# Kernel optimization log

Hardware: AMD Instinct MI355X
Metric: run time of the kernel (lower is better)

## Reference

```python
import jax, jax.numpy as jnp
import numpy as np

HDIM = 4
P = 2 ** HDIM  # 16 hypercube nodes


def build_dense_weight(hweight, out_features, in_features):
    # hweight: [hdim+1, P, ob, ib]; assemble dense [out_features, in_features]
    ob = out_features // P
    ib = in_features // P
    i = jnp.arange(P)
    w = jnp.zeros((P, P, ob, ib), dtype=hweight.dtype)
    # diagonal blocks: w[i, i] = hweight[0, i]
    w = w.at[i, i].set(hweight[0])
    # hypercube neighbor blocks: w[i ^ (1<<d), i] = hweight[d+1, i]
    for d in range(HDIM):
        j = i ^ (1 << d)
        w = w.at[j, i].set(hweight[d + 1])
    # permute (0,2,1,3) then reshape -> [out_features, in_features]
    w = jnp.transpose(w, (0, 2, 1, 3)).reshape(out_features, in_features)
    return w


def setup_inputs() -> dict:
    key = jax.random.key(0)
    k1, k2, k3 = jax.random.split(key, 3)
    in_features, out_features = 4096, 4096
    ob = out_features // P
    ib = in_features // P
    x = jax.random.normal(k1, (8192, in_features), dtype=jnp.float32)
    # kaiming-uniform-like scale for the block weights
    bound_w = 1.0 / np.sqrt(ib)
    hweight = jax.random.uniform(k2, (HDIM + 1, P, ob, ib), dtype=jnp.float32,
                                 minval=-bound_w, maxval=bound_w)
    bound_b = 1.0 / np.sqrt(in_features * (HDIM + 1))
    hbias = jax.random.uniform(k3, (out_features,), dtype=jnp.float32,
                               minval=-bound_b, maxval=bound_b)
    return {"x": x, "hweight": hweight, "hbias": hbias}


def reference(x, hweight, hbias):
    out_features = hweight.shape[1] * hweight.shape[2]
    in_features = hweight.shape[1] * hweight.shape[3]
    w = build_dense_weight(hweight, out_features, in_features)
    # F.linear(x, w, b) = x @ w.T + b
    return x @ w.T + hbias
```

## Files before the change

### kernel.cpp

```cpp
#include <hip/hip_runtime.h>

typedef __attribute__((ext_vector_type(8))) short short8;
typedef __attribute__((ext_vector_type(4))) float f32x4;

#define BM 128
#define BN 128
#define BK 32
#define INF 4096

#define AS1 __attribute__((address_space(1)))
#define AS3 __attribute__((address_space(3)))

__device__ __forceinline__ unsigned short f2bf(float f) {
    unsigned int u = __float_as_uint(f);
    u += 0x7FFFu + ((u >> 16) & 1u);
    return (unsigned short)(u >> 16);
}

__device__ __forceinline__ void gl_lds16(const unsigned short* g, unsigned short* l) {
    __builtin_amdgcn_global_load_lds((const AS1 void*)g, (AS3 void*)l, 16, 0, 0);
}

__global__ __launch_bounds__(256)
void cvt_bf16(const float* __restrict__ x, const float* __restrict__ hw,
              unsigned short* __restrict__ xb, unsigned short* __restrict__ wb)
{
    const long long NX = 8192LL * 4096;
    const long long NW = 5LL * 16 * 256 * 256;
    const long long total8 = (NX + NW) / 8;
    for (long long i = (long long)blockIdx.x * 256 + threadIdx.x; i < total8;
         i += (long long)gridDim.x * 256) {
        long long e = i * 8;
        const float* src;
        unsigned short* dst;
        long long off;
        if (e < NX) { src = x;  dst = xb; off = e; }
        else        { src = hw; dst = wb; off = e - NX; }
        float4 f0 = *(const float4*)(src + off);
        float4 f1 = *(const float4*)(src + off + 4);
        ushort4 u0, u1;
        u0.x = f2bf(f0.x); u0.y = f2bf(f0.y); u0.z = f2bf(f0.z); u0.w = f2bf(f0.w);
        u1.x = f2bf(f1.x); u1.y = f2bf(f1.y); u1.z = f2bf(f1.z); u1.w = f2bf(f1.w);
        *(ushort4*)(dst + off)     = u0;
        *(ushort4*)(dst + off + 4) = u1;
    }
}

__global__ __launch_bounds__(256)
void hcl_gemm(const unsigned short* __restrict__ xb,
              const unsigned short* __restrict__ wb,
              const float* __restrict__ hb,
              float* __restrict__ out)
{
    __shared__ unsigned short As[BM][BK];
    __shared__ unsigned short Bs[BN][BK];

    const int tid  = threadIdx.x;
    const int lane = tid & 63;
    const int wave = tid >> 6;
    const int wr   = wave >> 1, wc = wave & 1;

    const int bm0 = blockIdx.x * BM;
    const int p   = blockIdx.y >> 1;
    const int nh  = blockIdx.y & 1;

    f32x4 acc[4][4] = {};

    const int srow = tid >> 2;
    const int scol = (lane & 3) * 8;
    unsigned short* ldsA0 = &As[wave * 16][0];
    unsigned short* ldsA1 = &As[64 + wave * 16][0];
    unsigned short* ldsB0 = &Bs[wave * 16][0];
    unsigned short* ldsB1 = &Bs[64 + wave * 16][0];

    #pragma unroll
    for (int t = 0; t < 5; ++t) {
        const int mask = (t == 0) ? 0 : (1 << (t - 1));
        const int s = p ^ mask;
        const unsigned short* xc = xb + (size_t)bm0 * INF + s * 256;
        const unsigned short* wc_ = wb + ((size_t)(t * 16 + s) * 256 + nh * 128) * 256;

        for (int k8 = 0; k8 < 8; ++k8) {
            const int kc = k8 * BK;

            gl_lds16(xc  + (size_t)srow        * INF + kc + scol, ldsA0);
            gl_lds16(xc  + (size_t)(64 + srow) * INF + kc + scol, ldsA1);
            gl_lds16(wc_ + (size_t)srow        * 256 + kc + scol, ldsB0);
            gl_lds16(wc_ + (size_t)(64 + srow) * 256 + kc + scol, ldsB1);

            __syncthreads();

            short8 a[4], b[4];
            #pragma unroll
            for (int mi = 0; mi < 4; ++mi)
                a[mi] = *(const short8*)&As[wr * 64 + mi * 16 + (lane & 15)][(lane >> 4) * 8];
            #pragma unroll
            for (int nj = 0; nj < 4; ++nj)
                b[nj] = *(const short8*)&Bs[wc * 64 + nj * 16 + (lane & 15)][(lane >> 4) * 8];

            #pragma unroll
            for (int mi = 0; mi < 4; ++mi)
                #pragma unroll
                for (int nj = 0; nj < 4; ++nj)
                    acc[mi][nj] = __builtin_amdgcn_mfma_f32_16x16x32_bf16(
                        a[mi], b[nj], acc[mi][nj], 0, 0, 0);

            __syncthreads();
        }
    }

    const int col0 = p * 256 + nh * 128 + wc * 64;
    #pragma unroll
    for (int nj = 0; nj < 4; ++nj) {
        const int col = col0 + nj * 16 + (lane & 15);
        const float bias = hb[col];
        #pragma unroll
        for (int mi = 0; mi < 4; ++mi) {
            #pragma unroll
            for (int r = 0; r < 4; ++r) {
                const int row = bm0 + wr * 64 + mi * 16 + (lane >> 4) * 4 + r;
                out[(size_t)row * 4096 + col] = acc[mi][nj][r] + bias;
            }
        }
    }
}

__global__ __launch_bounds__(256)
void hcl_mfma_fused(const float* __restrict__ x,
                    const float* __restrict__ hw,
                    const float* __restrict__ hb,
                    float* __restrict__ out)
{
    __shared__ unsigned short As[BM][BK];
    __shared__ unsigned short Bs[BN][BK];

    const int tid  = threadIdx.x;
    const int lane = tid & 63;
    const int wave = tid >> 6;
    const int wr   = wave >> 1, wc = wave & 1;

    const int bm0 = blockIdx.x * BM;
    const int p   = blockIdx.y >> 1;
    const int nh  = blockIdx.y & 1;

    f32x4 acc[4][4] = {};

    const int srow = tid >> 3;
    const int scol = (tid & 7) * 4;

    #pragma unroll
    for (int t = 0; t < 5; ++t) {
        const int mask = (t == 0) ? 0 : (1 << (t - 1));
        const int s = p ^ mask;
        const float* xchunk = x  + (size_t)bm0 * INF + s * 256;
        const float* wchunk = hw + ((size_t)(t * 16 + s) * 256 + nh * 128) * 256;

        for (int k8 = 0; k8 < 8; ++k8) {
            const int kc = k8 * BK;
            #pragma unroll
            for (int i = 0; i < 4; ++i) {
                const int row = i * 32 + srow;
                float4 fa = *(const float4*)(xchunk + (size_t)row * INF + kc + scol);
                float4 fb = *(const float4*)(wchunk + (size_t)row * 256 + kc + scol);
                ushort4 ua, ub;
                ua.x = f2bf(fa.x); ua.y = f2bf(fa.y);
                ua.z = f2bf(fa.z); ua.w = f2bf(fa.w);
                ub.x = f2bf(fb.x); ub.y = f2bf(fb.y);
                ub.z = f2bf(fb.z); ub.w = f2bf(fb.w);
                *(ushort4*)&As[row][scol] = ua;
                *(ushort4*)&Bs[row][scol] = ub;
            }
            __syncthreads();

            short8 a[4], b[4];
            #pragma unroll
            for (int mi = 0; mi < 4; ++mi)
                a[mi] = *(const short8*)&As[wr * 64 + mi * 16 + (lane & 15)][(lane >> 4) * 8];
            #pragma unroll
            for (int nj = 0; nj < 4; ++nj)
                b[nj] = *(const short8*)&Bs[wc * 64 + nj * 16 + (lane & 15)][(lane >> 4) * 8];

            #pragma unroll
            for (int mi = 0; mi < 4; ++mi)
                #pragma unroll
                for (int nj = 0; nj < 4; ++nj)
                    acc[mi][nj] = __builtin_amdgcn_mfma_f32_16x16x32_bf16(
                        a[mi], b[nj], acc[mi][nj], 0, 0, 0);

            __syncthreads();
        }
    }

    const int col0 = p * 256 + nh * 128 + wc * 64;
    #pragma unroll
    for (int nj = 0; nj < 4; ++nj) {
        const int col = col0 + nj * 16 + (lane & 15);
        const float bias = hb[col];
        #pragma unroll
        for (int mi = 0; mi < 4; ++mi) {
            #pragma unroll
            for (int r = 0; r < 4; ++r) {
                const int row = bm0 + wr * 64 + mi * 16 + (lane >> 4) * 4 + r;
                out[(size_t)row * 4096 + col] = acc[mi][nj][r] + bias;
            }
        }
    }
}

extern "C" void kernel_launch(void* const* d_in, const int* in_sizes, int n_in,
                              void* d_out, int out_size, void* d_ws, size_t ws_size,
                              hipStream_t stream) {
    const float* x  = (const float*)d_in[0];
    const float* hw = (const float*)d_in[1];
    const float* hb = (const float*)d_in[2];
    float* out = (float*)d_out;

    const size_t NX = 8192ull * 4096;
    const size_t NW = 5ull * 16 * 256 * 256;
    const size_t need = (NX + NW) * sizeof(unsigned short);

    if (ws_size >= need) {
        unsigned short* xb = (unsigned short*)d_ws;
        unsigned short* wb = xb + NX;
        cvt_bf16<<<2048, 256, 0, stream>>>(x, hw, xb, wb);
        dim3 grid(8192 / BM, 32);
        hcl_gemm<<<grid, 256, 0, stream>>>(xb, wb, hb, out);
    } else {
        dim3 grid(8192 / BM, 32);
        hcl_mfma_fused<<<grid, 256, 0, stream>>>(x, hw, hb, out);
    }
}
```

Baseline: 169.2 us.

## Rewrite bf16 GEMM with 256x256 tiles, triple-buffered LDS and swizzle

```diff
diff --git a/kernel.cpp b/kernel.cpp
--- a/kernel.cpp
+++ b/kernel.cpp
@@ -3,10 +3,9 @@
 typedef __attribute__((ext_vector_type(8))) short short8;
 typedef __attribute__((ext_vector_type(4))) float f32x4;
 
-#define BM 128
-#define BN 128
-#define BK 32
 #define INF 4096
+#define NKT 40
+#define BUFB 32768
 
 #define AS1 __attribute__((address_space(1)))
 #define AS3 __attribute__((address_space(3)))
@@ -17,9 +16,11 @@
     return (unsigned short)(u >> 16);
 }
 
-__device__ __forceinline__ void gl_lds16(const unsigned short* g, unsigned short* l) {
+__device__ __forceinline__ void gl_lds16(const unsigned short* g, void* l) {
     __builtin_amdgcn_global_load_lds((const AS1 void*)g, (AS3 void*)l, 16, 0, 0);
 }
+
+__device__ __forceinline__ int swz(int b) { return b ^ ((b >> 3) & 0x30); }
 
 __global__ __launch_bounds__(256)
 void cvt_bf16(const float* __restrict__ x, const float* __restrict__ hw,
@@ -46,80 +47,108 @@
     }
 }
 
-__global__ __launch_bounds__(256)
-void hcl_gemm(const unsigned short* __restrict__ xb,
-              const unsigned short* __restrict__ wb,
-              const float* __restrict__ hb,
-              float* __restrict__ out)
+__global__ __launch_bounds__(512, 2)
+void hcl_gemm8(const unsigned short* __restrict__ xb,
+               const unsigned short* __restrict__ wb,
+               const float* __restrict__ hb,
+               float* __restrict__ out)
 {
-    __shared__ unsigned short As[BM][BK];
-    __shared__ unsigned short Bs[BN][BK];
+    extern __shared__ unsigned short lds[];
 
     const int tid  = threadIdx.x;
     const int lane = tid & 63;
     const int wave = tid >> 6;
-    const int wr   = wave >> 1, wc = wave & 1;
-
-    const int bm0 = blockIdx.x * BM;
-    const int p   = blockIdx.y >> 1;
-    const int nh  = blockIdx.y & 1;
-
-    f32x4 acc[4][4] = {};
-
-    const int srow = tid >> 2;
-    const int scol = (lane & 3) * 8;
-    unsigned short* ldsA0 = &As[wave * 16][0];
-    unsigned short* ldsA1 = &As[64 + wave * 16][0];
-    unsigned short* ldsB0 = &Bs[wave * 16][0];
-    unsigned short* ldsB1 = &Bs[64 + wave * 16][0];
-
-    #pragma unroll
-    for (int t = 0; t < 5; ++t) {
-        const int mask = (t == 0) ? 0 : (1 << (t - 1));
-        const int s = p ^ mask;
-        const unsigned short* xc = xb + (size_t)bm0 * INF + s * 256;
-        const unsigned short* wc_ = wb + ((size_t)(t * 16 + s) * 256 + nh * 128) * 256;
-
-        for (int k8 = 0; k8 < 8; ++k8) {
-            const int kc = k8 * BK;
-
-            gl_lds16(xc  + (size_t)srow        * INF + kc + scol, ldsA0);
-            gl_lds16(xc  + (size_t)(64 + srow) * INF + kc + scol, ldsA1);
-            gl_lds16(wc_ + (size_t)srow        * 256 + kc + scol, ldsB0);
-            gl_lds16(wc_ + (size_t)(64 + srow) * 256 + kc + scol, ldsB1);
-
-            __syncthreads();
-
-            short8 a[4], b[4];
-            #pragma unroll
-            for (int mi = 0; mi < 4; ++mi)
-                a[mi] = *(const short8*)&As[wr * 64 + mi * 16 + (lane & 15)][(lane >> 4) * 8];
-            #pragma unroll
-            for (int nj = 0; nj < 4; ++nj)
-                b[nj] = *(const short8*)&Bs[wc * 64 + nj * 16 + (lane & 15)][(lane >> 4) * 8];
-
-            #pragma unroll
-            for (int mi = 0; mi < 4; ++mi)
-                #pragma unroll
-                for (int nj = 0; nj < 4; ++nj)
-                    acc[mi][nj] = __builtin_amdgcn_mfma_f32_16x16x32_bf16(
-                        a[mi], b[nj], acc[mi][nj], 0, 0, 0);
-
-            __syncthreads();
-        }
-    }
-
-    const int col0 = p * 256 + nh * 128 + wc * 64;
-    #pragma unroll
-    for (int nj = 0; nj < 4; ++nj) {
-        const int col = col0 + nj * 16 + (lane & 15);
+    const int wr   = wave >> 2;
+    const int wcn  = wave & 3;
+    const int ln15 = lane & 15;
+    const int hi   = lane >> 4;
+
+    const int bm0 = blockIdx.x * 256;
+    const int p   = blockIdx.y;
+
+    const int b0 = tid * 16;
+    const int b1 = (512 + tid) * 16;
+    const int g0 = swz(b0), g1 = swz(b1);
+    const int rS0 = g0 >> 6, cS0 = (g0 & 63) >> 1;
+    const int rS1 = g1 >> 6, cS1 = (g1 & 63) >> 1;
+
+    int offA[8], offB[4];
+    #pragma unroll
+    for (int mf = 0; mf < 8; ++mf) {
+        int row = wr * 128 + mf * 16 + ln15;
+        offA[mf] = swz(row * 64 + hi * 16);
+    }
+    #pragma unroll
+    for (int nf = 0; nf < 4; ++nf) {
+        int row = wcn * 64 + nf * 16 + ln15;
+        offB[nf] = swz(row * 64 + hi * 16);
+    }
+
+    f32x4 acc[8][4] = {};
+
+    auto STAGE = [&](int kt, int buf) {
+        const int t = kt >> 3;
+        const int s = p ^ ((1 << t) >> 1);
+        const unsigned short* ga = xb + (size_t)bm0 * INF + s * 256 + (kt & 7) * 32;
+        const unsigned short* gb = wb + ((size_t)(t * 16 + s) << 16) + (kt & 7) * 32;
+        char* lb = (char*)lds + buf * BUFB + wave * 1024;
+        gl_lds16(ga + (size_t)rS0 * INF + cS0, lb);
+        gl_lds16(ga + (size_t)rS1 * INF + cS1, lb + 8192);
+        gl_lds16(gb + (size_t)rS0 * 256 + cS0, lb + 16384);
+        gl_lds16(gb + (size_t)rS1 * 256 + cS1, lb + 16384 + 8192);
+    };
+
+    auto COMPUTE = [&](int buf) {
+        const char* LA = (const char*)lds + buf * BUFB;
+        const char* LB = LA + 16384;
+        short8 fa[8], fb[4];
+        #pragma unroll
+        for (int nf = 0; nf < 4; ++nf) fb[nf] = *(const short8*)(LB + offB[nf]);
+        #pragma unroll
+        for (int mf = 0; mf < 8; ++mf) fa[mf] = *(const short8*)(LA + offA[mf]);
+        __builtin_amdgcn_s_setprio(1);
+        #pragma unroll
+        for (int mf = 0; mf < 8; ++mf)
+            #pragma unroll
+            for (int nf = 0; nf < 4; ++nf)
+                acc[mf][nf] = __builtin_amdgcn_mfma_f32_16x16x32_bf16(
+                    fa[mf], fb[nf], acc[mf][nf], 0, 0, 0);
+        __builtin_amdgcn_s_setprio(0);
+    };
+
+    STAGE(0, 0);
+    STAGE(1, 1);
+
+    for (int kt = 0; kt < NKT - 2; ++kt) {
+        STAGE(kt + 2, (kt + 2) % 3);
+        asm volatile("s_waitcnt vmcnt(8)");
+        __builtin_amdgcn_s_barrier();
+        __builtin_amdgcn_sched_barrier(0);
+        COMPUTE(kt % 3);
+        __builtin_amdgcn_s_barrier();
+        __builtin_amdgcn_sched_barrier(0);
+    }
+    asm volatile("s_waitcnt vmcnt(4)");
+    __builtin_amdgcn_s_barrier();
+    __builtin_amdgcn_sched_barrier(0);
+    COMPUTE((NKT - 2) % 3);
+    __builtin_amdgcn_s_barrier();
+    asm volatile("s_waitcnt vmcnt(0)");
+    __builtin_amdgcn_s_barrier();
+    __builtin_amdgcn_sched_barrier(0);
+    COMPUTE((NKT - 1) % 3);
+
+    const int col0 = p * 256 + wcn * 64;
+    #pragma unroll
+    for (int nf = 0; nf < 4; ++nf) {
+        const int col = col0 + nf * 16 + ln15;
         const float bias = hb[col];
         #pragma unroll
-        for (int mi = 0; mi < 4; ++mi) {
+        for (int mf = 0; mf < 8; ++mf) {
             #pragma unroll
             for (int r = 0; r < 4; ++r) {
-                const int row = bm0 + wr * 64 + mi * 16 + (lane >> 4) * 4 + r;
-                out[(size_t)row * 4096 + col] = acc[mi][nj][r] + bias;
+                const int row = bm0 + wr * 128 + mf * 16 + hi * 4 + r;
+                out[(size_t)row * 4096 + col] = acc[mf][nf][r] + bias;
             }
         }
     }
@@ -131,15 +160,15 @@
                     const float* __restrict__ hb,
                     float* __restrict__ out)
 {
-    __shared__ unsigned short As[BM][BK];
-    __shared__ unsigned short Bs[BN][BK];
+    __shared__ unsigned short As[128][32];
+    __shared__ unsigned short Bs[128][32];
 
     const int tid  = threadIdx.x;
     const int lane = tid & 63;
     const int wave = tid >> 6;
     const int wr   = wave >> 1, wc = wave & 1;
 
-    const int bm0 = blockIdx.x * BM;
+    const int bm0 = blockIdx.x * 128;
     const int p   = blockIdx.y >> 1;
     const int nh  = blockIdx.y & 1;
 
@@ -156,7 +185,7 @@
         const float* wchunk = hw + ((size_t)(t * 16 + s) * 256 + nh * 128) * 256;
 
         for (int k8 = 0; k8 < 8; ++k8) {
-            const int kc = k8 * BK;
+            const int kc = k8 * 32;
             #pragma unroll
             for (int i = 0; i < 4; ++i) {
                 const int row = i * 32 + srow;
@@ -223,10 +252,10 @@
         unsigned short* xb = (unsigned short*)d_ws;
         unsigned short* wb = xb + NX;
         cvt_bf16<<<2048, 256, 0, stream>>>(x, hw, xb, wb);
-        dim3 grid(8192 / BM, 32);
-        hcl_gemm<<<grid, 256, 0, stream>>>(xb, wb, hb, out);
+        dim3 grid(8192 / 256, 16);
+        hcl_gemm8<<<grid, 512, 3 * BUFB, stream>>>(xb, wb, hb, out);
     } else {
-        dim3 grid(8192 / BM, 32);
+        dim3 grid(8192 / 128, 32);
         hcl_mfma_fused<<<grid, 256, 0, stream>>>(x, hw, hb, out);
     }
 }
```

Result: faster. 154.4 us (-8.8%).
